# Optimization experiments

Measured on AMD Instinct MI355X. Metric: run time of the kernel, lower is better.

## Reference

```python
import jax, jax.numpy as jnp
import numpy as np
import math

PATCHSIZE = [(64, 64), (32, 32), (16, 16), (8, 8)]


def conv2d(x, w, bias, padding, dilation=1):
    # x: [N,C,H,W], w: [O,I,kh,kw]
    y = jax.lax.conv_general_dilated(
        x, w, window_strides=(1, 1),
        padding=[(padding, padding), (padding, padding)],
        rhs_dilation=(dilation, dilation),
        dimension_numbers=('NCHW', 'OIHW', 'NCHW'))
    return y + bias[None, :, None, None]


def lrelu(x):
    return jnp.where(x >= 0, x, 0.2 * x)


def to_windows(z, b, t, d_k, out_h, hh, out_w, ww):
    # z: [b*t, d_k, h, w] -> [b, t*out_h*out_w, d_k*hh*ww]
    z = z.reshape(b, t, d_k, out_h, hh, out_w, ww)
    z = z.transpose(0, 1, 3, 5, 2, 4, 6)
    return z.reshape(b, t * out_h * out_w, d_k * hh * ww)


def from_windows(y, b, t, d_k, out_h, hh, out_w, ww):
    # inverse of to_windows -> [b*t, d_k, h, w]
    y = y.reshape(b, t, out_h, out_w, d_k, hh, ww)
    y = y.transpose(0, 1, 4, 2, 5, 3, 6)
    return y.reshape(b * t, d_k, out_h * hh, out_w * ww)


def setup_inputs() -> dict:
    key = jax.random.key(0)
    ks = jax.random.split(key, 12)
    bt, c, h, w = 16, 128, 128, 128
    g = 0.02
    inp = {
        'x': jax.random.normal(ks[0], (bt, c, h, w), jnp.float32),
        'Wq': g * jax.random.normal(ks[1], (c, c, 1, 1), jnp.float32),
        'bq': jnp.zeros((c,), jnp.float32),
        'Wk': g * jax.random.normal(ks[2], (c, c, 1, 1), jnp.float32),
        'bk': jnp.zeros((c,), jnp.float32),
        'Wv': g * jax.random.normal(ks[3], (c, c, 1, 1), jnp.float32),
        'bv': jnp.zeros((c,), jnp.float32),
        'Wo': g * jax.random.normal(ks[4], (c, c, 3, 3), jnp.float32),
        'bo': jnp.zeros((c,), jnp.float32),
        'Wf1': g * jax.random.normal(ks[5], (c, c, 3, 3), jnp.float32),
        'bf1': jnp.zeros((c,), jnp.float32),
        'Wf2': g * jax.random.normal(ks[6], (c, c, 3, 3), jnp.float32),
        'bf2': jnp.zeros((c,), jnp.float32),
        'b': 4,
        'c': 128,
    }
    return inp


def reference(x, Wq, bq, Wk, bk, Wv, bv, Wo, bo, Wf1, bf1, Wf2, bf2, b, c):
    bt, _, h, w = x.shape
    t = bt // b
    n_ps = len(PATCHSIZE)
    d_k = c // n_ps

    x0 = x
    q_all = conv2d(x, Wq, bq, padding=0)
    k_all = conv2d(x, Wk, bk, padding=0)
    v_all = conv2d(x, Wv, bv, padding=0)

    outs = []
    for i, (ww_, hh_) in enumerate(PATCHSIZE):  # (width, height)
        sl = slice(i * d_k, (i + 1) * d_k)
        out_w, out_h = w // ww_, h // hh_
        q = to_windows(q_all[:, sl], b, t, d_k, out_h, hh_, out_w, ww_)
        k = to_windows(k_all[:, sl], b, t, d_k, out_h, hh_, out_w, ww_)
        v = to_windows(v_all[:, sl], b, t, d_k, out_h, hh_, out_w, ww_)
        dim = q.shape[-1]
        scores = jnp.einsum('bnd,bmd->bnm', q, k) / math.sqrt(dim)
        p = jax.nn.softmax(scores, axis=-1)
        y = jnp.einsum('bnm,bmd->bnd', p, v)
        outs.append(from_windows(y, b, t, d_k, out_h, hh_, out_w, ww_))

    attn = jnp.concatenate(outs, axis=1)  # [bt, c, h, w]
    attn = lrelu(conv2d(attn, Wo, bo, padding=1))
    x = x0 + attn
    ff = lrelu(conv2d(x, Wf1, bf1, padding=2, dilation=2))
    ff = lrelu(conv2d(ff, Wf2, bf2, padding=1))
    return x + ff
```

## Files before the change

### kernel.cpp

```cpp
#include <hip/hip_runtime.h>
#include <stdint.h>

#define C_   128
#define H_   128
#define W_   128
#define HW_  (128*128)

#define SC_OFF3 0
#define SC_OFF2 4194304
#define SC_OFF1 4456448
#define SC_OFF0 4472832
#define SC_TOT  4473856

typedef unsigned short ushort_t;
typedef __attribute__((ext_vector_type(8)))  short bf16x8;
typedef __attribute__((ext_vector_type(16))) float f32x16;

__device__ __forceinline__ float bf2f(uint32_t u) {
    union { float f; uint32_t i; } v; v.i = u << 16; return v.f;
}
__device__ __forceinline__ uint32_t f2bf(float f) {
    union { float f; uint32_t i; } v; v.f = f;
    uint32_t u = v.i;
    uint32_t r = u + 0x7FFFu + ((u >> 16) & 1u);
    return r >> 16;
}
__device__ __forceinline__ void async16(const ushort_t* g, void* l) {
    __builtin_amdgcn_global_load_lds(
        (const __attribute__((address_space(1))) unsigned int*)g,
        (__attribute__((address_space(3))) unsigned int*)l, 16, 0, 0);
}


__global__ __launch_bounds__(256) void prepack_kernel(
    const float* __restrict__ Wo, const float* __restrict__ Wf1,
    const float* __restrict__ Wf2, ushort_t* __restrict__ Wp)
{
    int t = blockIdx.x * 256 + threadIdx.x;
    const float* W = (blockIdx.y == 0) ? Wo : ((blockIdx.y == 1) ? Wf1 : Wf2);
    ushort_t* dst = Wp + (size_t)blockIdx.y * 147456;
    int j = t & 7, lane = (t >> 3) & 63, f = t >> 9;
    int cot = f & 3, s = (f >> 2) & 1, tap = (f >> 3) % 9, cc = f / 72;
    int co = cot * 32 + (lane & 31);
    int ci = cc * 32 + s * 16 + (lane >> 5) * 8 + j;
    dst[t] = (ushort_t)f2bf(W[((size_t)co * 128 + ci) * 9 + tap]);
}

__global__ __launch_bounds__(256) void prepack1_kernel(
    const float* __restrict__ Wq, const float* __restrict__ Wk,
    const float* __restrict__ Wv, ushort_t* __restrict__ Wqkv)
{
    int t = blockIdx.x * 256 + threadIdx.x;
    const float* W = (blockIdx.y == 0) ? Wq : ((blockIdx.y == 1) ? Wk : Wv);
    ushort_t* dst = Wqkv + (size_t)blockIdx.y * 16384;
    int j = t & 7, lane = (t >> 3) & 63, f = t >> 9;
    int cot = f & 3, s = f >> 2;
    int co = cot * 32 + (lane & 31);
    int ci = s * 16 + (lane >> 5) * 8 + j;
    dst[t] = (ushort_t)f2bf(W[(size_t)co * 128 + ci]);
}

__global__ __launch_bounds__(256) void nchw2nhwc_kernel(
    const float* __restrict__ in, ushort_t* __restrict__ out)
{
    __shared__ ushort_t tile[128 * 136];
    const int img = blockIdx.y, hh = blockIdx.x;
    const int tid = threadIdx.x;
    #pragma unroll
    for (int i = 0; i < 8; ++i) {
        int idx = tid + 256 * i;
        int c = idx >> 4, w8 = (idx & 15) * 8;
        size_t src = ((size_t)img * 128 + c) * (size_t)HW_ + hh * 128 + w8;
        const float4* fp = (const float4*)&in[src];
        float4 f0 = fp[0], f1 = fp[1];
        ushort_t v[8];
        v[0] = (ushort_t)f2bf(f0.x); v[1] = (ushort_t)f2bf(f0.y);
        v[2] = (ushort_t)f2bf(f0.z); v[3] = (ushort_t)f2bf(f0.w);
        v[4] = (ushort_t)f2bf(f1.x); v[5] = (ushort_t)f2bf(f1.y);
        v[6] = (ushort_t)f2bf(f1.z); v[7] = (ushort_t)f2bf(f1.w);
        #pragma unroll
        for (int k = 0; k < 8; ++k) {
            int w = w8 + k;
            int g = (c >> 3) ^ ((w >> 3) & 7);
            tile[w * 136 + g * 8 + (c & 7)] = v[k];
        }
    }
    __syncthreads();
    #pragma unroll
    for (int i = 0; i < 8; ++i) {
        int idx = tid + 256 * i;
        int w = idx >> 4, g = idx & 15;
        int gs = g ^ ((w >> 3) & 7);
        uint4 raw = *(const uint4*)&tile[w * 136 + gs * 8];
        int c8 = g * 8;
        size_t off = (((size_t)(img * 128 + hh)) * 8 + (c8 >> 4)) * 2048 + w * 16 + (c8 & 8);
        *(uint4*)&out[off] = raw;
    }
}

__global__ __launch_bounds__(256) void attn2nhwc_kernel(
    const ushort_t* __restrict__ in, ushort_t* __restrict__ out)
{
    __shared__ ushort_t tile[128 * 136];
    const int img = blockIdx.y, hh = blockIdx.x;
    const int tid = threadIdx.x;
    #pragma unroll
    for (int i = 0; i < 8; ++i) {
        int idx = tid + 256 * i;
        int c = idx >> 4, w8 = (idx & 15) * 8;
        size_t src = (((size_t)((c >> 5) * 16 + img)) * 32 + (c & 31)) * (size_t)HW_
                     + hh * 128 + w8;
        uint4 raw = *(const uint4*)&in[src];
        ushort_t v[8];
        v[0] = raw.x & 0xffffu; v[1] = raw.x >> 16;
        v[2] = raw.y & 0xffffu; v[3] = raw.y >> 16;
        v[4] = raw.z & 0xffffu; v[5] = raw.z >> 16;
        v[6] = raw.w & 0xffffu; v[7] = raw.w >> 16;
        #pragma unroll
        for (int k = 0; k < 8; ++k) {
            int w = w8 + k;
            int g = (c >> 3) ^ ((w >> 3) & 7);
            tile[w * 136 + g * 8 + (c & 7)] = v[k];
        }
    }
    __syncthreads();
    #pragma unroll
    for (int i = 0; i < 8; ++i) {
        int idx = tid + 256 * i;
        int w = idx >> 4, g = idx & 15;
        int gs = g ^ ((w >> 3) & 7);
        uint4 raw = *(const uint4*)&tile[w * 136 + gs * 8];
        int c8 = g * 8;
        size_t off = (((size_t)(img * 128 + hh)) * 8 + (c8 >> 4)) * 2048 + w * 16 + (c8 & 8);
        *(uint4*)&out[off] = raw;
    }
}

__global__ __launch_bounds__(768, 1) void qkvm_kernel(
    const ushort_t* __restrict__ xn, const ushort_t* __restrict__ Wqkv,
    const float* __restrict__ bq, const float* __restrict__ bk,
    const float* __restrict__ bv,
    ushort_t* __restrict__ qw, ushort_t* __restrict__ kw,
    ushort_t* __restrict__ vw)
{
    __shared__ ushort_t lds[24576];
    const int h = blockIdx.x, img = blockIdx.y;
    const int tid = threadIdx.x, lane = tid & 63, wv = tid >> 6;
    const int w3 = wv >> 2, iw = wv & 3;
    const int pxh = iw & 1, coh = iw >> 1;
    const int kch = lane >> 5;
    const ushort_t* Wb = Wqkv + (size_t)w3 * 16384;
    const float* bias = (w3 == 0) ? bq : ((w3 == 1) ? bk : bv);
    const int b_ = img >> 2, t_ = img & 3;

    f32x16 acc[2][2];
    #pragma unroll
    for (int i = 0; i < 2; ++i)
        #pragma unroll
        for (int j = 0; j < 2; ++j)
            #pragma unroll
            for (int k = 0; k < 16; ++k) acc[i][j][k] = 0.f;

    auto STAGE = [&](int p, int b) {
        if (w3 == 0) {
            int kb = iw;
            int px = kb * 32 + (lane >> 1), ch = lane & 1;
            int cg = ch ^ ((px >> 2) & 1);
            const ushort_t* src = xn + (((size_t)(img * 128 + h)) * 8 + p) * 2048
                                  + px * 16 + cg * 8;
            async16(src, (char*)lds + b * 4096 + kb * 1024);
        }
    };

    STAGE(0, 0);
    STAGE(1, 1);
    #pragma unroll
    for (int p = 0; p < 8; ++p) {
        const int fbase = p * 4 + coh * 2;
        bf16x8 wa0 = *(const bf16x8*)(Wb + ((size_t)fbase * 64 + lane) * 8);
        bf16x8 wa1 = *(const bf16x8*)(Wb + ((size_t)(fbase + 1) * 64 + lane) * 8);
        asm volatile("" ::: "memory");
        if (p < 6) STAGE(p + 2, (p + 2) % 3);
        if (p < 6)      asm volatile("s_waitcnt vmcnt(4)" ::: "memory");
        else if (p == 6) asm volatile("s_waitcnt vmcnt(3)" ::: "memory");
        else             asm volatile("s_waitcnt vmcnt(2)" ::: "memory");
        __builtin_amdgcn_s_barrier();
        __builtin_amdgcn_s_setprio(1);
        const ushort_t* bbuf = lds + (p % 3) * 2048;
        #pragma unroll
        for (int i = 0; i < 2; ++i) {
            int px = pxh * 64 + i * 32 + (lane & 31);
            int s = kch ^ ((px >> 2) & 1);
            bf16x8 bv4 = *(const bf16x8*)(bbuf + px * 16 + s * 8);
            acc[i][0] = __builtin_amdgcn_mfma_f32_32x32x16_bf16(wa0, bv4, acc[i][0], 0, 0, 0);
            acc[i][1] = __builtin_amdgcn_mfma_f32_32x32x16_bf16(wa1, bv4, acc[i][1], 0, 0, 0);
        }
        __builtin_amdgcn_s_setprio(0);
        __builtin_amdgcn_s_barrier();
    }

    #pragma unroll
    for (int j = 0; j < 2; ++j) {
        __syncthreads();
        {
            const int scale = coh * 2 + j;
            ushort_t* tile = lds + w3 * 8192 + coh * 4096;
            #pragma unroll
            for (int rg = 0; rg < 16; ++rg) {
                int c_local = (rg & 3) + 8 * (rg >> 2) + 4 * kch;
                float bb = bias[scale * 32 + c_local];
                #pragma unroll
                for (int i = 0; i < 2; ++i) {
                    int px = pxh * 64 + i * 32 + (lane & 31);
                    tile[c_local * 128 + px] = (ushort_t)f2bf(acc[i][j][rg] + bb);
                }
            }
        }
        __syncthreads();
        #pragma unroll
        for (int l = 0; l < 4; ++l) {
            int idx = l * 768 + tid;
            int g3 = idx >> 10, rem = idx & 1023;
            int coh_t = rem >> 9, rem2 = rem & 511;
            int c_local = rem2 >> 4, r8 = rem2 & 15;
            int px0 = r8 * 8;
            int scale = coh_t * 2 + j;
            int lg = 6 - scale;
            int psz = 1 << lg, outn = 128 >> lg;
            int Dd = 32 << (2 * lg);
            int oh = h >> lg, ph = h & (psz - 1);
            int ow = px0 >> lg, pw0 = px0 & (psz - 1);
            ushort_t* outp = (g3 == 0) ? qw : ((g3 == 1) ? kw : vw);
            size_t off = (size_t)scale * 8388608u
                + ((size_t)((b_ * 4 + t_) * outn * outn + oh * outn)) * (size_t)Dd
                + (size_t)ow * Dd + (size_t)(((c_local << lg) + ph) << lg) + pw0;
            uint4 raw = *(const uint4*)&lds[g3 * 8192 + coh_t * 4096 + c_local * 128 + px0];
            *(uint4*)&outp[off] = raw;
        }
    }
}

__device__ __forceinline__ void vtrans_dev(
    const ushort_t* __restrict__ src, ushort_t* __restrict__ dst,
    int n, int Dd, int xb, int yb, int b_)
{
    const int ddb = xb * 128, tokb = yb * 128;
    const int tid = threadIdx.x;
    const int ti = tid & 15, tj = tid >> 4;
    const int tok0 = tokb + ti * 8, dd0 = ddb + tj * 8;
    if (tok0 >= n) return;
    const ushort_t* s = src + (size_t)b_ * (size_t)n * Dd;
    ushort_t* d = dst + (size_t)b_ * (size_t)n * Dd;
    ushort_t a[8][8];
    #pragma unroll
    for (int e = 0; e < 8; ++e)
        *(uint4*)a[e] = *(const uint4*)&s[(size_t)(tok0 + e) * Dd + dd0];
    #pragma unroll
    for (int q = 0; q < 8; ++q) {
        ushort_t o[8];
        #pragma unroll
        for (int e = 0; e < 8; ++e) o[e] = a[e][q];
        *(uint4*)&d[(size_t)(dd0 + q) * n + tok0] = *(uint4*)o;
    }
}

__global__ __launch_bounds__(256) void vtrans_all_kernel(
    const ushort_t* __restrict__ vw, ushort_t* __restrict__ vt)
{
    const int bid = blockIdx.x;
    if (bid < 4096) {
        int sid = bid;
        vtrans_dev(vw + 0u, vt + 0u, 16, 131072, sid & 1023, 0, sid >> 10);
    } else if (bid < 5120) {
        int sid = bid - 4096;
        vtrans_dev(vw + 8388608u, vt + 8388608u, 64, 32768, sid & 255, 0, sid >> 8);
    } else if (bid < 5632) {
        int sid = bid - 5120;
        vtrans_dev(vw + 16777216u, vt + 16777216u, 256, 8192, sid & 63, (sid >> 6) & 1, sid >> 7);
    } else {
        int sid = bid - 5632;
        vtrans_dev(vw + 25165824u, vt + 25165824u, 1024, 2048, sid & 15, (sid >> 4) & 7, sid >> 7);
    }
}

template<int LG, int KS>
__device__ __forceinline__ void scores_lds_dev(
    const ushort_t* __restrict__ qw, const ushort_t* __restrict__ kw,
    float* __restrict__ sc_s, int bx, int by, int b_, int ks, ushort_t* lds)
{
    constexpr int outn = 128 >> LG;
    constexpr int n = 4 * outn * outn;
    constexpr int Dd = 32 << (2 * LG);
    constexpr int scale = 6 - LG;
    constexpr int DdK = Dd / KS;
    constexpr int NPH = DdK / 64;
    const size_t base = (size_t)scale * 8388608u;
    const int tid = threadIdx.x, lane = tid & 63, wv = tid >> 6;
    const ushort_t* qb = qw + base + (size_t)b_ * (size_t)n * Dd;
    const ushort_t* kb = kw + base + (size_t)b_ * (size_t)n * Dd;
    float* scb = sc_s + (size_t)b_ * n * n;
    const float scl = rsqrtf((float)Dd);
    const int mb = bx * 128, nb = by * 128;
    const int mbl = (wv & 1) * 64, nbl = (wv >> 1) * 64;
    const int k0beg = ks * DdK;

    f32x16 acc[2][2];
    #pragma unroll
    for (int i = 0; i < 2; ++i)
        #pragma unroll
        for (int j = 0; j < 2; ++j)
            #pragma unroll
            for (int k = 0; k < 16; ++k) acc[i][j][k] = 0.f;

    auto STAGE = [&](int k0, int buf) {
        #pragma unroll
        for (int l = 0; l < 4; ++l) {
            int id = l * 256 + tid;
            int row = id >> 3, ch = id & 7;
            int sw = ch ^ (row & 7);
            async16(qb + (size_t)(mb + row) * Dd + k0 + sw * 8,
                    (char*)lds + buf * 32768 + id * 16);
        }
        #pragma unroll
        for (int l = 0; l < 4; ++l) {
            int id = l * 256 + tid;
            int row = id >> 3, ch = id & 7;
            int sw = ch ^ (row & 7);
            async16(kb + (size_t)(nb + row) * Dd + k0 + sw * 8,
                    (char*)lds + buf * 32768 + 16384 + id * 16);
        }
    };

    STAGE(k0beg, 0);
    for (int p = 0; p < NPH; ++p) {
        if (p + 1 < NPH) STAGE(k0beg + (p + 1) * 64, (p + 1) & 1);
        if (p + 1 < NPH) asm volatile("s_waitcnt vmcnt(8)" ::: "memory");
        else             asm volatile("s_waitcnt vmcnt(0)" ::: "memory");
        __builtin_amdgcn_s_barrier();
        __builtin_amdgcn_s_setprio(1);
        const ushort_t* bufA = lds + (p & 1) * 16384;
        const ushort_t* bufB = bufA + 8192;
        #pragma unroll
        for (int u = 0; u < 4; ++u) {
            const int c = u * 2 + (lane >> 5);
            bf16x8 a[2], b[2];
            #pragma unroll
            for (int i = 0; i < 2; ++i) {
                int row = mbl + i * 32 + (lane & 31);
                a[i] = *(const bf16x8*)(bufA + row * 64 + ((c ^ (row & 7)) << 3));
            }
            #pragma unroll
            for (int j = 0; j < 2; ++j) {
                int row = nbl + j * 32 + (lane & 31);
                b[j] = *(const bf16x8*)(bufB + row * 64 + ((c ^ (row & 7)) << 3));
            }
            #pragma unroll
            for (int i = 0; i < 2; ++i)
                #pragma unroll
                for (int j = 0; j < 2; ++j)
                    acc[i][j] = __builtin_amdgcn_mfma_f32_32x32x16_bf16(a[i], b[j], acc[i][j], 0, 0, 0);
        }
        __builtin_amdgcn_s_setprio(0);
        __builtin_amdgcn_s_barrier();
    }

    #pragma unroll
    for (int i = 0; i < 2; ++i)
        #pragma unroll
        for (int j = 0; j < 2; ++j)
            #pragma unroll
            for (int rg = 0; rg < 16; ++rg) {
                int row = mb + mbl + i * 32 + (rg & 3) + 8 * (rg >> 2) + 4 * (lane >> 5);
                int col = nb + nbl + j * 32 + (lane & 31);
                float v = acc[i][j][rg] * scl;
                size_t off = (size_t)row * n + col;
                if (KS == 1) scb[off] = v;
                else atomicAdd(&scb[off], v);
            }
}

template<int CFG, int LG, int KS>
__device__ __forceinline__ void scores_dev(
    const ushort_t* __restrict__ qw, const ushort_t* __restrict__ kw,
    float* __restrict__ sc_s, int b_, int ks)
{
    constexpr int outn = 128 >> LG;
    constexpr int n = 4 * outn * outn;
    constexpr int Dd = 32 << (2 * LG);
    constexpr int scale = 6 - LG;
    constexpr int DdK = Dd / KS;
    const size_t base = (size_t)scale * 8388608u;
    const int tid = threadIdx.x, lane = tid & 63, wv = tid >> 6;
    const ushort_t* qb = qw + base + (size_t)b_ * (size_t)n * Dd;
    const ushort_t* kb = kw + base + (size_t)b_ * (size_t)n * Dd;
    float* scb = sc_s + (size_t)b_ * n * n;
    const float scl = rsqrtf((float)Dd);
    const int koff = (lane >> 5) * 8;
    const int mbq = (CFG == 1) ? (wv & 1) * 32 : 0;
    const int nbq = (CFG == 1) ? (wv >> 1) * 32 : 0;

    f32x16 acc;
    #pragma unroll
    for (int k = 0; k < 16; ++k) acc[k] = 0.f;

    int mrow = mbq + (lane & 31);
    int nrow = nbq + (lane & 31);
    if (CFG == 2) { if (mrow >= n) mrow = n - 1; if (nrow >= n) nrow = n - 1; }
    int k0beg = ks * DdK, k0end = k0beg + DdK;
    if (CFG == 2) { constexpr int DdW = DdK >> 2; k0beg += wv * DdW; k0end = k0beg + DdW; }

    for (int k0 = k0beg; k0 < k0end; k0 += 64) {
        bf16x8 a[4], b[4];
        #pragma unroll
        for (int u = 0; u < 4; ++u) {
            a[u] = *(const bf16x8*)(qb + (size_t)mrow * Dd + k0 + u * 16 + koff);
            b[u] = *(const bf16x8*)(kb + (size_t)nrow * Dd + k0 + u * 16 + koff);
        }
        #pragma unroll
        for (int u = 0; u < 4; ++u)
            acc = __builtin_amdgcn_mfma_f32_32x32x16_bf16(a[u], b[u], acc, 0, 0, 0);
    }

    #pragma unroll
    for (int rg = 0; rg < 16; ++rg) {
        int row = mbq + (rg & 3) + 8 * (rg >> 2) + 4 * (lane >> 5);
        int col = nbq + (lane & 31);
        if (CFG == 2 && (row >= n || col >= n)) continue;
        float v = acc[rg] * scl;
        size_t off = (size_t)row * n + col;
        atomicAdd(&scb[off], v);
    }
}

__global__ __launch_bounds__(256, 2) void scores_all_kernel(
    const ushort_t* __restrict__ qw, const ushort_t* __restrict__ kw,
    float* __restrict__ sc)
{
    __shared__ ushort_t slds[32768];
    const int bid = blockIdx.x;
    if (bid < 256) {
        int l = bid;            int sid = (l & 7) * 32 + (l >> 3);
        scores_lds_dev<3, 1>(qw, kw, sc + SC_OFF3, sid & 7, (sid >> 3) & 7, sid >> 6, 0, slds);
    } else if (bid < 512) {
        int l = bid - 256;      int sid = (l & 7) * 32 + (l >> 3);
        scores_lds_dev<4, 16>(qw, kw, sc + SC_OFF2, sid & 1, (sid >> 1) & 1, sid >> 6, (sid >> 2) & 15, slds);
    } else if (bid < 768) {
        int l = bid - 512;      int sid = (l & 7) * 32 + (l >> 3);
        scores_dev<1, 5, 64>(qw, kw, sc + SC_OFF1, sid >> 6, sid & 63);
    } else {
        int l = bid - 768;      int sid = (l & 7) * 32 + (l >> 3);
        scores_dev<2, 6, 64>(qw, kw, sc + SC_OFF0, sid >> 6, sid & 63);
    }
}

__global__ __launch_bounds__(256) void softmax_all_kernel(
    const float* __restrict__ sc, ushort_t* __restrict__ pbf)
{
    const int bid = blockIdx.x;
    int n; size_t off; int row;
    if (bid < 64)        { n = 16;   row = bid;        off = SC_OFF0; }
    else if (bid < 320)  { n = 64;   row = bid - 64;   off = SC_OFF1; }
    else if (bid < 1344) { n = 256;  row = bid - 320;  off = SC_OFF2; }
    else                 { n = 1024; row = bid - 1344; off = SC_OFF3; }
    const float* p = sc + off + (size_t)row * n;
    ushort_t* q = pbf + off + (size_t)row * n;
    const int tid = threadIdx.x;
    float v[4];
    #pragma unroll
    for (int j = 0; j < 4; ++j) { int idx = tid + 256 * j; v[j] = (idx < n) ? p[idx] : -3.0e38f; }
    float m = fmaxf(fmaxf(v[0], v[1]), fmaxf(v[2], v[3]));
    #pragma unroll
    for (int off2 = 32; off2 >= 1; off2 >>= 1) m = fmaxf(m, __shfl_xor(m, off2));
    __shared__ float red[4];
    const int wid = tid >> 6, lane = tid & 63;
    if (lane == 0) red[wid] = m;
    __syncthreads();
    m = fmaxf(fmaxf(red[0], red[1]), fmaxf(red[2], red[3]));
    float e[4]; float s = 0.f;
    #pragma unroll
    for (int j = 0; j < 4; ++j) { int idx = tid + 256 * j; e[j] = (idx < n) ? __expf(v[j] - m) : 0.f; s += e[j]; }
    #pragma unroll
    for (int off2 = 32; off2 >= 1; off2 >>= 1) s += __shfl_xor(s, off2);
    __syncthreads();
    if (lane == 0) red[wid] = s;
    __syncthreads();
    s = red[0] + red[1] + red[2] + red[3];
    float inv = 1.0f / s;
    #pragma unroll
    for (int j = 0; j < 4; ++j) {
        int idx = tid + 256 * j;
        if (idx < n) q[idx] = (ushort_t)f2bf(e[j] * inv);
    }
}

template<int LG>
__device__ __forceinline__ void pvm_lds_dev(
    const ushort_t* __restrict__ pbf_s, const ushort_t* __restrict__ vt,
    ushort_t* __restrict__ attn, int bx, int by, int b_, ushort_t* lds)
{
    constexpr int outn = 128 >> LG, psz = 1 << LG;
    constexpr int n = 4 * outn * outn;
    constexpr int Dd = 32 << (2 * LG);
    constexpr int scale = 6 - LG;
    constexpr int NPH = n / 64;
    const int tid = threadIdx.x, lane = tid & 63, wv = tid >> 6;
    const ushort_t* pb = pbf_s + (size_t)b_ * n * n;
    const ushort_t* vb = vt + (size_t)scale * 8388608u + (size_t)b_ * (size_t)Dd * n;
    const int mb = by * 128;
    const int nb = bx * 128;
    const int mbl = (wv & 1) * 64, nbl = (wv >> 1) * 64;

    f32x16 acc[2][2];
    #pragma unroll
    for (int i = 0; i < 2; ++i)
        #pragma unroll
        for (int j = 0; j < 2; ++j)
            #pragma unroll
            for (int k = 0; k < 16; ++k) acc[i][j][k] = 0.f;

    auto STAGE = [&](int k0, int buf) {
        #pragma unroll
        for (int l = 0; l < 4; ++l) {
            int id = l * 256 + tid;
            int row = id >> 3, ch = id & 7;
            int sw = ch ^ (row & 7);
            async16(pb + (size_t)(mb + row) * n + k0 + sw * 8,
                    (char*)lds + buf * 32768 + id * 16);
        }
        #pragma unroll
        for (int l = 0; l < 4; ++l) {
            int id = l * 256 + tid;
            int row = id >> 3, ch = id & 7;
            int sw = ch ^ (row & 7);
            async16(vb + (size_t)(nb + row) * n + k0 + sw * 8,
                    (char*)lds + buf * 32768 + 16384 + id * 16);
        }
    };

    STAGE(0, 0);
    for (int p = 0; p < NPH; ++p) {
        if (p + 1 < NPH) STAGE((p + 1) * 64, (p + 1) & 1);
        if (p + 1 < NPH) asm volatile("s_waitcnt vmcnt(8)" ::: "memory");
        else             asm volatile("s_waitcnt vmcnt(0)" ::: "memory");
        __builtin_amdgcn_s_barrier();
        __builtin_amdgcn_s_setprio(1);
        const ushort_t* bufA = lds + (p & 1) * 16384;
        const ushort_t* bufB = bufA + 8192;
        #pragma unroll
        for (int u = 0; u < 4; ++u) {
            const int c = u * 2 + (lane >> 5);
            bf16x8 a[2], b[2];
            #pragma unroll
            for (int i = 0; i < 2; ++i) {
                int row = mbl + i * 32 + (lane & 31);
                a[i] = *(const bf16x8*)(bufA + row * 64 + ((c ^ (row & 7)) << 3));
            }
            #pragma unroll
            for (int j = 0; j < 2; ++j) {
                int row = nbl + j * 32 + (lane & 31);
                b[j] = *(const bf16x8*)(bufB + row * 64 + ((c ^ (row & 7)) << 3));
            }
            #pragma unroll
            for (int i = 0; i < 2; ++i)
                #pragma unroll
                for (int j = 0; j < 2; ++j)
                    acc[i][j] = __builtin_amdgcn_mfma_f32_32x32x16_bf16(a[i], b[j], acc[i][j], 0, 0, 0);
        }
        __builtin_amdgcn_s_setprio(0);
        __builtin_amdgcn_s_barrier();
    }

    constexpr int lgo = 7 - LG;
    #pragma unroll
    for (int i = 0; i < 2; ++i)
        #pragma unroll
        for (int j = 0; j < 2; ++j)
            #pragma unroll
            for (int rg = 0; rg < 16; ++rg) {
                int tok = mb + mbl + i * 32 + (rg & 3) + 8 * (rg >> 2) + 4 * (lane >> 5);
                int dd = nb + nbl + j * 32 + (lane & 31);
                int c_local = dd >> (2 * LG);
                int p2 = dd & (psz * psz - 1);
                int ph = p2 >> LG, pw = p2 & (psz - 1);
                int t_ = tok >> (2 * lgo);
                int rem = tok & ((1 << (2 * lgo)) - 1);
                int oh = rem >> lgo, ow = rem & (outn - 1);
                size_t off = (((size_t)(scale * 16 + b_ * 4 + t_) * 32 + c_local) * 128
                              + ((oh << LG) + ph)) * 128 + ((ow << LG) + pw);
                attn[off] = (ushort_t)f2bf(acc[i][j][rg]);
            }
}

template<int CFG, int LG>
__device__ __forceinline__ void pvm_dev(
    const ushort_t* __restrict__ pbf_s, const ushort_t* __restrict__ vt,
    ushort_t* __restrict__ attn, int bx, int by, int b_)
{
    constexpr int outn = 128 >> LG, psz = 1 << LG;
    constexpr int n = 4 * outn * outn;
    constexpr int Dd = 32 << (2 * LG);
    constexpr int scale = 6 - LG;
    const int tid = threadIdx.x, lane = tid & 63, wv = tid >> 6;
    const ushort_t* pb = pbf_s + (size_t)b_ * n * n;
    const ushort_t* vb = vt + (size_t)scale * 8388608u + (size_t)b_ * (size_t)Dd * n;
    const int mb = (CFG == 1) ? (wv & 1) * 32 : 0;
    const int nb = (CFG == 1) ? bx * 128 + (wv >> 1) * 64
                              : bx * 256 + wv * 64;
    const int koff = (lane >> 5) * 8;

    f32x16 acc[2];
    #pragma unroll
    for (int j = 0; j < 2; ++j)
        #pragma unroll
        for (int k = 0; k < 16; ++k) acc[j][k] = 0.f;

    int mr = mb + (lane & 31);
    if (CFG == 2 && mr >= n) mr = n - 1;
    const int nr0 = nb + (lane & 31), nr1 = nr0 + 32;

    if constexpr (CFG == 2) {
        bf16x8 b0 = *(const bf16x8*)(vb + (size_t)nr0 * n + koff);
        bf16x8 b1 = *(const bf16x8*)(vb + (size_t)nr1 * n + koff);
        bf16x8 a = *(const bf16x8*)(pb + (size_t)mr * n + koff);
        acc[0] = __builtin_amdgcn_mfma_f32_32x32x16_bf16(a, b0, acc[0], 0, 0, 0);
        acc[1] = __builtin_amdgcn_mfma_f32_32x32x16_bf16(a, b1, acc[1], 0, 0, 0);
    } else {
        for (int k0 = 0; k0 < n; k0 += 64) {
            bf16x8 vb0[4], vb1[4], pa[4];
            #pragma unroll
            for (int u = 0; u < 4; ++u) {
                vb0[u] = *(const bf16x8*)(vb + (size_t)nr0 * n + k0 + u * 16 + koff);
                vb1[u] = *(const bf16x8*)(vb + (size_t)nr1 * n + k0 + u * 16 + koff);
                pa[u]  = *(const bf16x8*)(pb + (size_t)mr * n + k0 + u * 16 + koff);
            }
            #pragma unroll
            for (int u = 0; u < 4; ++u) {
                acc[0] = __builtin_amdgcn_mfma_f32_32x32x16_bf16(pa[u], vb0[u], acc[0], 0, 0, 0);
                acc[1] = __builtin_amdgcn_mfma_f32_32x32x16_bf16(pa[u], vb1[u], acc[1], 0, 0, 0);
            }
        }
    }

    constexpr int lgo = 7 - LG;
    #pragma unroll
    for (int j = 0; j < 2; ++j)
        #pragma unroll
        for (int rg = 0; rg < 16; ++rg) {
            int tok = mb + (rg & 3) + 8 * (rg >> 2) + 4 * (lane >> 5);
            if (CFG == 2 && tok >= n) continue;
            int dd = nb + j * 32 + (lane & 31);
            int c_local = dd >> (2 * LG);
            int p2 = dd & (psz * psz - 1);
            int ph = p2 >> LG, pw = p2 & (psz - 1);
            int t_ = tok >> (2 * lgo);
            int rem = tok & ((1 << (2 * lgo)) - 1);
            int oh = rem >> lgo, ow = rem & (outn - 1);
            size_t off = (((size_t)(scale * 16 + b_ * 4 + t_) * 32 + c_local) * 128
                          + ((oh << LG) + ph)) * 128 + ((ow << LG) + pw);
            attn[off] = (ushort_t)f2bf(acc[j][rg]);
        }
}

__global__ __launch_bounds__(256, 2) void pvm_all_kernel(
    const ushort_t* __restrict__ pbf, const ushort_t* __restrict__ vt,
    ushort_t* __restrict__ attn)
{
    __shared__ ushort_t plds[32768];
    const int bid = blockIdx.x;
    if (bid < 512) {
        int l = bid;            int sid = (l & 7) * 64 + (l >> 3);
        pvm_lds_dev<3>(pbf + SC_OFF3, vt, attn, sid & 15, (sid >> 4) & 7, sid >> 7, plds);
    } else if (bid < 1024) {
        int l = bid - 512;      int sid = (l & 7) * 64 + (l >> 3);
        pvm_lds_dev<4>(pbf + SC_OFF2, vt, attn, sid & 63, (sid >> 6) & 1, sid >> 7, plds);
    } else if (bid < 2048) {
        int l = bid - 1024;     int sid = (l & 7) * 128 + (l >> 3);
        pvm_dev<1, 5>(pbf + SC_OFF1, vt, attn, sid & 255, 0, sid >> 8);
    } else {
        int l = bid - 2048;     int sid = (l & 7) * 256 + (l >> 3);
        pvm_dev<2, 6>(pbf + SC_OFF0, vt, attn, sid & 511, 0, sid >> 9);
    }
}

template<int DIL, int MODE>
__global__ __launch_bounds__(256, 2) void conv3x_kernel(
    const ushort_t* __restrict__ in, const ushort_t* __restrict__ Wp,
    const float* __restrict__ bias, const ushort_t* __restrict__ resn,
    float* __restrict__ outf, ushort_t* __restrict__ outn,
    const ushort_t* __restrict__ zp)
{
    __shared__ ushort_t lds[34816];
    const int fid = blockIdx.y * 64 + blockIdx.x;
    const int nfid = (fid & 7) * 128 + (fid >> 3);
    const int img = nfid >> 6, rp = nfid & 63;
    const int h0 = (DIL == 1) ? rp * 2 : ((rp & 1) + (rp >> 1) * 4);
    const int tid = threadIdx.x, lane = tid & 63, wv = tid >> 6;
    const int pxh = wv & 1, coq = wv >> 1;
    const int kch = lane >> 5;

    f32x16 acc[2][2][2];
    #pragma unroll
    for (int r = 0; r < 2; ++r)
        #pragma unroll
        for (int i = 0; i < 2; ++i)
            #pragma unroll
            for (int j = 0; j < 2; ++j)
                #pragma unroll
                for (int k = 0; k < 16; ++k) acc[r][i][j][k] = 0.f;

    auto STAGE = [&](int p, int b) {
        #pragma unroll
        for (int kb = wv; kb < 20; kb += 4) {
            int slot = kb / 5, pg = kb % 5;
            int pxi = pg * 32 + (lane >> 1);
            int wc = pxi - 16;
            int ir = h0 - DIL + slot * DIL;
            int cg = (lane & 1) ^ ((pxi >> 2) & 1);
            const ushort_t* src;
            if (wc >= 0 && wc < 128 && ir >= 0 && ir < 128)
                src = in + (((size_t)(img * 128 + ir)) * 8 + p) * 2048 + wc * 16 + cg * 8;
            else
                src = zp + lane * 8;
            async16(src, (char*)lds + b * 20480 + kb * 1024);
        }
    };

    STAGE(0, 0);
    #pragma unroll
    for (int p = 0; p < 8; ++p) {
        bf16x8 w0[9], w1[9];
        #pragma unroll
        for (int tap = 0; tap < 9; ++tap) {
            int fbase = (((p >> 1) * 9 + tap) * 2 + (p & 1)) * 4 + coq * 2;
            w0[tap] = *(const bf16x8*)(Wp + ((size_t)fbase * 64 + lane) * 8);
            w1[tap] = *(const bf16x8*)(Wp + ((size_t)(fbase + 1) * 64 + lane) * 8);
        }
        asm volatile("" ::: "memory");
        if (p < 7) STAGE(p + 1, (p + 1) & 1);
        if (p < 7) asm volatile("s_waitcnt vmcnt(23)" ::: "memory");
        else       asm volatile("s_waitcnt vmcnt(18)" ::: "memory");
        __builtin_amdgcn_s_barrier();
        __builtin_amdgcn_s_setprio(1);
        const ushort_t* bbuf = lds + (p & 1) * 10240;
        #pragma unroll
        for (int tap = 0; tap < 9; ++tap) {
            const int tr = tap / 3, tc = tap % 3;
            #pragma unroll
            for (int r = 0; r < 2; ++r) {
                const ushort_t* sb = bbuf + (r + tr) * 2560;
                #pragma unroll
                for (int i = 0; i < 2; ++i) {
                    int pxi = pxh * 64 + i * 32 + (lane & 31) + (tc - 1) * DIL + 16;
                    int s = kch ^ ((pxi >> 2) & 1);
                    bf16x8 bv = *(const bf16x8*)(sb + pxi * 16 + s * 8);
                    acc[r][i][0] = __builtin_amdgcn_mfma_f32_32x32x16_bf16(w0[tap], bv, acc[r][i][0], 0, 0, 0);
                    acc[r][i][1] = __builtin_amdgcn_mfma_f32_32x32x16_bf16(w1[tap], bv, acc[r][i][1], 0, 0, 0);
                }
            }
        }
        __builtin_amdgcn_s_setprio(0);
        __builtin_amdgcn_s_barrier();
    }
    __syncthreads();

    if (MODE == 0 || MODE == 2) {
        #pragma unroll
        for (int r = 0; r < 2; ++r) {
            const int hr = h0 + r * DIL;
            for (int u = tid; u < 2048; u += 256) {
                int px = u >> 4, c8 = (u & 15) * 8;
                size_t soff = (((size_t)(img * 128 + hr)) * 8 + (c8 >> 4)) * 2048 + px * 16 + (c8 & 8);
                *(uint4*)&lds[r * 17408 + px * 136 + c8] = *(const uint4*)&resn[soff];
            }
        }
        __syncthreads();
    }
    #pragma unroll
    for (int r = 0; r < 2; ++r) {
        const int hr = h0 + r * DIL;
        #pragma unroll
        for (int i = 0; i < 2; ++i)
            #pragma unroll
            for (int tn = 0; tn < 2; ++tn)
                #pragma unroll
                for (int rgq = 0; rgq < 4; ++rgq) {
                    const int cob = coq * 64 + tn * 32 + 8 * rgq + 4 * kch;
                    const int px = pxh * 64 + i * 32 + (lane & 31);
                    float v[4];
                    #pragma unroll
                    for (int e = 0; e < 4; ++e) {
                        float t = acc[r][i][tn][rgq * 4 + e] + bias[cob + e];
                        v[e] = (t >= 0.f) ? t : 0.2f * t;
                    }
                    if (MODE == 0) {
                        uint2 rr = *(const uint2*)&lds[r * 17408 + px * 136 + cob];
                        float w0v = bf2f(rr.x & 0xffffu) + v[0];
                        float w1v = bf2f(rr.x >> 16)     + v[1];
                        float w2v = bf2f(rr.y & 0xffffu) + v[2];
                        float w3v = bf2f(rr.y >> 16)     + v[3];
                        uint2 pk;
                        pk.x = f2bf(w0v) | (f2bf(w1v) << 16);
                        pk.y = f2bf(w2v) | (f2bf(w3v) << 16);
                        *(uint2*)&lds[r * 17408 + px * 136 + cob] = pk;
                    } else if (MODE == 1) {
                        uint2 pk;
                        pk.x = f2bf(v[0]) | (f2bf(v[1]) << 16);
                        pk.y = f2bf(v[2]) | (f2bf(v[3]) << 16);
                        *(uint2*)&lds[r * 17408 + px * 136 + cob] = pk;
                    } else {
                        uint2 rr = *(const uint2*)&lds[r * 17408 + px * 136 + cob];
                        float rv[4] = { bf2f(rr.x & 0xffffu), bf2f(rr.x >> 16),
                                        bf2f(rr.y & 0xffffu), bf2f(rr.y >> 16) };
                        #pragma unroll
                        for (int e = 0; e < 4; ++e)
                            outf[(((size_t)(img * 128 + cob + e)) * 128 + hr) * 128 + px] = rv[e] + v[e];
                    }
                }
    }
    if (MODE == 0 || MODE == 1) {
        __syncthreads();
        #pragma unroll
        for (int r = 0; r < 2; ++r) {
            const int hr = h0 + r * DIL;
            for (int u = tid; u < 2048; u += 256) {
                int px = u >> 4, c8 = (u & 15) * 8;
                size_t doff = (((size_t)(img * 128 + hr)) * 8 + (c8 >> 4)) * 2048 + px * 16 + (c8 & 8);
                *(uint4*)&outn[doff] = *(const uint4*)&lds[r * 17408 + px * 136 + c8];
            }
        }
    }
}

extern "C" void kernel_launch(void* const* d_in, const int* in_sizes, int n_in,
                              void* d_out, int out_size, void* d_ws, size_t ws_size,
                              hipStream_t stream)
{
    const float* x   = (const float*)d_in[0];
    const float* Wq  = (const float*)d_in[1];
    const float* bq  = (const float*)d_in[2];
    const float* Wk  = (const float*)d_in[3];
    const float* bk  = (const float*)d_in[4];
    const float* Wv  = (const float*)d_in[5];
    const float* bv  = (const float*)d_in[6];
    const float* Wo  = (const float*)d_in[7];
    const float* bo  = (const float*)d_in[8];
    const float* Wf1 = (const float*)d_in[9];
    const float* bf1 = (const float*)d_in[10];
    const float* Wf2 = (const float*)d_in[11];
    const float* bf2 = (const float*)d_in[12];
    float* out = (float*)d_out;
    char* ws = (char*)d_ws;
    const size_t MB = 1048576ull;
    ushort_t* qw   = (ushort_t*)(ws);
    ushort_t* kw   = (ushort_t*)(ws + 64 * MB);
    ushort_t* vw   = (ushort_t*)(ws + 128 * MB);
    ushort_t* xn   = (ushort_t*)(ws + 192 * MB);
    float*    sc   = (float*)   (ws + 256 * MB);
    ushort_t* Wp   = (ushort_t*)(ws + 274 * MB);
    ushort_t* Wqkv = (ushort_t*)(ws + 275 * MB);
    ushort_t* zp   = (ushort_t*)(ws + 275 * MB + 256 * 1024);
    ushort_t* pbf  = (ushort_t*)(ws + 276 * MB);
    ushort_t* attnc = qw;
    ushort_t* vt    = kw;
    ushort_t* nhwc  = vw;
    ushort_t* x1n   = kw;
    ushort_t* ff1n  = qw;

    hipMemsetAsync(zp, 0, 1024, stream);
    hipMemsetAsync(sc + SC_OFF2, 0, (size_t)(SC_TOT - SC_OFF2) * 4, stream);
    prepack_kernel<<<dim3(576, 3), 256, 0, stream>>>(Wo, Wf1, Wf2, Wp);
    prepack1_kernel<<<dim3(64, 3), 256, 0, stream>>>(Wq, Wk, Wv, Wqkv);

    nchw2nhwc_kernel<<<dim3(128, 16), 256, 0, stream>>>(x, xn);
    qkvm_kernel<<<dim3(128, 16), 768, 0, stream>>>(xn, Wqkv, bq, bk, bv, qw, kw, vw);

    scores_all_kernel<<<dim3(1024), 256, 0, stream>>>(qw, kw, sc);
    vtrans_all_kernel<<<dim3(6144), 256, 0, stream>>>(vw, vt);
    softmax_all_kernel<<<dim3(5440), 256, 0, stream>>>(sc, pbf);
    pvm_all_kernel<<<dim3(4096), 256, 0, stream>>>(pbf, vt, attnc);

    attn2nhwc_kernel<<<dim3(128, 16), 256, 0, stream>>>(attnc, nhwc);
    conv3x_kernel<1, 0><<<dim3(64, 16), 256, 0, stream>>>(nhwc, Wp, bo, xn, nullptr, x1n, zp);
    conv3x_kernel<2, 1><<<dim3(64, 16), 256, 0, stream>>>(x1n, Wp + 147456, bf1, nullptr, nullptr, ff1n, zp);
    conv3x_kernel<1, 2><<<dim3(64, 16), 256, 0, stream>>>(ff1n, Wp + 2 * 147456, bf2, x1n, out, nullptr, zp);
}
```

Before: 666.8 us.

## Permute windowed Q/K/V feature order to (ph, c, pw) for contiguous row writes

Reorders the per-window feature dimension from (channel, ph, pw) to (ph, channel, pw), so each image row a QKV block produces lands as a contiguous span per window. The LDS staging tile gets a padded stride of 136 to reduce bank conflicts. The attention output kernels' index decoding is updated to match the new order. Dot products over the feature dimension do not depend on its order, so attention results are unchanged while global stores become more contiguous. The cost is a slightly larger LDS footprint.

Measured after the change: 630.2 us. 1.06x faster.

```diff
diff --git a/kernel.cpp b/kernel.cpp
--- a/kernel.cpp
+++ b/kernel.cpp
@@ -143,7 +143,7 @@
     ushort_t* __restrict__ qw, ushort_t* __restrict__ kw,
     ushort_t* __restrict__ vw)
 {
-    __shared__ ushort_t lds[24576];
+    __shared__ ushort_t lds[26112];
     const int h = blockIdx.x, img = blockIdx.y;
     const int tid = threadIdx.x, lane = tid & 63, wv = tid >> 6;
     const int w3 = wv >> 2, iw = wv & 3;
@@ -204,7 +204,7 @@
         __syncthreads();
         {
             const int scale = coh * 2 + j;
-            ushort_t* tile = lds + w3 * 8192 + coh * 4096;
+            ushort_t* tile = lds + (w3 * 2 + coh) * 4352;
             #pragma unroll
             for (int rg = 0; rg < 16; ++rg) {
                 int c_local = (rg & 3) + 8 * (rg >> 2) + 4 * kch;
@@ -212,7 +212,7 @@
                 #pragma unroll
                 for (int i = 0; i < 2; ++i) {
                     int px = pxh * 64 + i * 32 + (lane & 31);
-                    tile[c_local * 128 + px] = (ushort_t)f2bf(acc[i][j][rg] + bb);
+                    tile[c_local * 136 + px] = (ushort_t)f2bf(acc[i][j][rg] + bb);
                 }
             }
         }
@@ -222,19 +222,21 @@
             int idx = l * 768 + tid;
             int g3 = idx >> 10, rem = idx & 1023;
             int coh_t = rem >> 9, rem2 = rem & 511;
-            int c_local = rem2 >> 4, r8 = rem2 & 15;
-            int px0 = r8 * 8;
             int scale = coh_t * 2 + j;
             int lg = 6 - scale;
-            int psz = 1 << lg, outn = 128 >> lg;
+            int ow = rem2 >> (lg + 2);
+            int rem3 = rem2 & ((1 << (lg + 2)) - 1);
+            int c_local = rem3 >> (lg - 3);
+            int pw0 = (rem3 & ((1 << (lg - 3)) - 1)) << 3;
+            int outn = 128 >> lg;
             int Dd = 32 << (2 * lg);
-            int oh = h >> lg, ph = h & (psz - 1);
-            int ow = px0 >> lg, pw0 = px0 & (psz - 1);
+            int oh = h >> lg, ph = h & ((1 << lg) - 1);
             ushort_t* outp = (g3 == 0) ? qw : ((g3 == 1) ? kw : vw);
             size_t off = (size_t)scale * 8388608u
-                + ((size_t)((b_ * 4 + t_) * outn * outn + oh * outn)) * (size_t)Dd
-                + (size_t)ow * Dd + (size_t)(((c_local << lg) + ph) << lg) + pw0;
-            uint4 raw = *(const uint4*)&lds[g3 * 8192 + coh_t * 4096 + c_local * 128 + px0];
+                + ((size_t)((b_ * 4 + t_) * outn * outn + oh * outn + ow)) * (size_t)Dd
+                + ((size_t)ph << (lg + 5)) + (c_local << lg) + pw0;
+            uint4 raw = *(const uint4*)&lds[(g3 * 2 + coh_t) * 4352 + c_local * 136
+                                            + (ow << lg) + pw0];
             *(uint4*)&outp[off] = raw;
         }
     }
@@ -579,9 +581,10 @@
             for (int rg = 0; rg < 16; ++rg) {
                 int tok = mb + mbl + i * 32 + (rg & 3) + 8 * (rg >> 2) + 4 * (lane >> 5);
                 int dd = nb + nbl + j * 32 + (lane & 31);
-                int c_local = dd >> (2 * LG);
-                int p2 = dd & (psz * psz - 1);
-                int ph = p2 >> LG, pw = p2 & (psz - 1);
+                int ph = dd >> (LG + 5);
+                int r2 = dd & ((1 << (LG + 5)) - 1);
+                int c_local = r2 >> LG;
+                int pw = r2 & (psz - 1);
                 int t_ = tok >> (2 * lgo);
                 int rem = tok & ((1 << (2 * lgo)) - 1);
                 int oh = rem >> lgo, ow = rem & (outn - 1);
@@ -649,9 +652,10 @@
             int tok = mb + (rg & 3) + 8 * (rg >> 2) + 4 * (lane >> 5);
             if (CFG == 2 && tok >= n) continue;
             int dd = nb + j * 32 + (lane & 31);
-            int c_local = dd >> (2 * LG);
-            int p2 = dd & (psz * psz - 1);
-            int ph = p2 >> LG, pw = p2 & (psz - 1);
+            int ph = dd >> (LG + 5);
+            int r2 = dd & ((1 << (LG + 5)) - 1);
+            int c_local = r2 >> LG;
+            int pw = r2 & (psz - 1);
             int t_ = tok >> (2 * lgo);
             int rem = tok & ((1 << (2 * lgo)) - 1);
             int oh = rem >> lgo, ow = rem & (outn - 1);
```
